# Optimization experiments

Hardware: AMD Instinct MI355X
Metric: run time of the kernel (lower is better)

Reference implementation:

```python
import jax, jax.numpy as jnp
import numpy as np

B, S, E = 2, 2048, 1024
H = 16
D = E // H
LAYER_IDX = 2.0
MASKED_BIAS = -10000.0


def setup_inputs() -> dict:
    key = jax.random.key(0)
    k1, k2, k3 = jax.random.split(key, 3)
    hidden_state = jax.random.normal(k1, (B, S, E), dtype=jnp.float32)
    w_attn = jax.random.normal(k2, (E, 3 * E), dtype=jnp.float32) * 0.2
    b_attn = jnp.zeros((3 * E,), dtype=jnp.float32)
    w_proj = jax.random.normal(k3, (E, E), dtype=jnp.float32) * 0.2
    b_proj = jnp.zeros((E,), dtype=jnp.float32)
    return {"hidden_state": hidden_state, "w_attn": w_attn, "b_attn": b_attn,
            "w_proj": w_proj, "b_proj": b_proj}


def reference(hidden_state, w_attn, b_attn, w_proj, b_proj):
    b, s, e = hidden_state.shape
    # c_attn: Conv1D == x @ W + b, then split into q, k, v
    qkv = hidden_state @ w_attn + b_attn          # [b, s, 3E]
    q, k, v = jnp.split(qkv, 3, axis=-1)
    # split heads -> [b, H, s, D]
    def split_heads(t):
        return t.reshape(b, s, H, D).transpose(0, 2, 1, 3)
    q, k, v = split_heads(q), split_heads(k), split_heads(v)
    # QK^T scaled by sqrt(d_head) then by layer_idx
    scores = jnp.einsum("bhqd,bhkd->bhqk", q, k)
    scores = scores / jnp.asarray(D ** 0.5, scores.dtype)
    scores = scores / LAYER_IDX
    # causal mask with masked_bias fill (-10000.0), matching bias buffer slice
    causal = jnp.tril(jnp.ones((s, s), dtype=bool))  # [s, s]
    scores = jnp.where(causal[None, None, :, :], scores, jnp.asarray(MASKED_BIAS, scores.dtype))
    attn = jax.nn.softmax(scores, axis=-1)
    out = jnp.einsum("bhqk,bhkd->bhqd", attn, v)   # [b, H, s, D]
    # merge heads
    out = out.transpose(0, 2, 1, 3).reshape(b, s, e)
    # c_proj
    return out @ w_proj + b_proj
```

## Files before the change

kernel.cpp:

```cpp
#include <hip/hip_runtime.h>
#include <cstddef>
#include <cstdint>

#define B_DIM   2
#define S_LEN   2048
#define EMB     1024
#define NH      16
#define HD      64
#define QKV_N   3072
#define MROWS   (B_DIM * S_LEN)

using half8  = __attribute__((ext_vector_type(8))) _Float16;
using half4  = __attribute__((ext_vector_type(4))) _Float16;
using f32x4  = __attribute__((ext_vector_type(4))) float;

#if defined(__has_builtin)
#if __has_builtin(__builtin_amdgcn_global_load_lds)
#define HAS_GLL 1
#endif
#endif

__device__ __forceinline__ void stage16(const _Float16* g, _Float16* lds_base, int lane)
{
#ifdef HAS_GLL
    (void)lane;
    __builtin_amdgcn_global_load_lds(
        (const __attribute__((address_space(1))) unsigned int*)g,
        (__attribute__((address_space(3))) unsigned int*)lds_base, 16, 0, 0);
#else
    *(half8*)(lds_base + lane * 8) = *(const half8*)g;
#endif
}

__global__ __launch_bounds__(256)
void cast_f32_f16(const float* __restrict__ src, _Float16* __restrict__ dst)
{
    int i = (blockIdx.x * 256 + threadIdx.x) * 4;
    float4 v = *(const float4*)(src + i);
    half4 h = { (_Float16)v.x, (_Float16)v.y, (_Float16)v.z, (_Float16)v.w };
    *(half4*)(dst + i) = h;
}

__global__ __launch_bounds__(256)
void transpose_cast(const float* __restrict__ W, _Float16* __restrict__ Wt,
                    int K, int N)
{
    __shared__ float T[32][33];
    const int n0 = blockIdx.x * 32, k0 = blockIdx.y * 32;
    const int t = threadIdx.x;
    const int r = t >> 3, c4 = (t & 7) * 4;
    float4 w = *(const float4*)(W + (size_t)(k0 + r) * N + n0 + c4);
    T[r][c4 + 0] = w.x; T[r][c4 + 1] = w.y;
    T[r][c4 + 2] = w.z; T[r][c4 + 3] = w.w;
    __syncthreads();
    half4 h = { (_Float16)T[c4 + 0][r], (_Float16)T[c4 + 1][r],
                (_Float16)T[c4 + 2][r], (_Float16)T[c4 + 3][r] };
    *(half4*)(Wt + (size_t)(n0 + r) * K + k0 + c4) = h;
}

__global__ __launch_bounds__(256)
void transpose_v(const _Float16* __restrict__ qkv, _Float16* __restrict__ vt)
{
    __shared__ _Float16 T[64][66];
    const int st = blockIdx.x, bh = blockIdx.y;
    const int b = bh >> 4, h = bh & 15;
    const int t = threadIdx.x;
    const int sr = t >> 2, dc = (t & 3) * 16;

    const _Float16* src = qkv + ((size_t)(b * S_LEN + st * 64 + sr)) * QKV_N
                              + 2 * EMB + h * HD + dc;
    half8 v0 = *(const half8*)(src);
    half8 v1 = *(const half8*)(src + 8);
#pragma unroll
    for (int j = 0; j < 8; ++j) { T[sr][dc + j] = v0[j]; T[sr][dc + 8 + j] = v1[j]; }
    __syncthreads();

    const int dr = t >> 2, sc = (t & 3) * 16;
    half8 o0, o1;
#pragma unroll
    for (int j = 0; j < 8; ++j) { o0[j] = T[sc + j][dr]; o1[j] = T[sc + 8 + j][dr]; }
    _Float16* dst = vt + (size_t)bh * HD * S_LEN + (size_t)dr * S_LEN + st * 64 + sc;
    *(half8*)(dst)     = o0;
    *(half8*)(dst + 8) = o1;
}

template <int MT, int MINW, bool OUT_F16>
__global__ __launch_bounds__(256, MINW)
void hgemm_lds(const _Float16* __restrict__ X, const _Float16* __restrict__ Wt,
               const float* __restrict__ bias, void* __restrict__ Cout,
               int M, int N, int K)
{
    constexpr int BM = MT * 32;
    constexpr int CA = BM / 64;
    __shared__ _Float16 As[BM][32];
    __shared__ _Float16 Bs[128][32];

    const int tid  = threadIdx.x;
    const int wave = tid >> 6, lane = tid & 63;
    const int quad = lane >> 4, l15 = lane & 15;
    const int wm = (wave >> 1) * (MT * 16);
    const int wn = (wave & 1) * 64;
    const int m0 = blockIdx.y * BM, n0 = blockIdx.x * 128;

    const int lrow = lane >> 2;
    const int lcol = (lane & 3) * 8;

    const _Float16* xg[CA];
#pragma unroll
    for (int t = 0; t < CA; ++t)
        xg[t] = X + (size_t)(m0 + t * 64 + wave * 16 + lrow) * K + lcol;
    const _Float16* wg[2];
#pragma unroll
    for (int t = 0; t < 2; ++t)
        wg[t] = Wt + (size_t)(n0 + t * 64 + wave * 16 + lrow) * K + lcol;

    f32x4 acc[MT][4] = {};

    for (int k0 = 0; k0 < K; k0 += 32) {
#pragma unroll
        for (int t = 0; t < CA; ++t)
            stage16(xg[t] + k0, &As[t * 64 + wave * 16][0], lane);
#pragma unroll
        for (int t = 0; t < 2; ++t)
            stage16(wg[t] + k0, &Bs[t * 64 + wave * 16][0], lane);
        __syncthreads();

        half8 af[MT], bf[4];
#pragma unroll
        for (int mt = 0; mt < MT; ++mt)
            af[mt] = *(const half8*)&As[wm + mt * 16 + l15][quad * 8];
#pragma unroll
        for (int nt = 0; nt < 4; ++nt)
            bf[nt] = *(const half8*)&Bs[wn + nt * 16 + l15][quad * 8];
#pragma unroll
        for (int mt = 0; mt < MT; ++mt)
#pragma unroll
            for (int nt = 0; nt < 4; ++nt)
                acc[mt][nt] = __builtin_amdgcn_mfma_f32_16x16x32_f16(
                    af[mt], bf[nt], acc[mt][nt], 0, 0, 0);
        __syncthreads();
    }

#pragma unroll
    for (int nt = 0; nt < 4; ++nt) {
        const int c = n0 + wn + nt * 16 + l15;
        const float bv = bias[c];
#pragma unroll
        for (int mt = 0; mt < MT; ++mt)
#pragma unroll
            for (int reg = 0; reg < 4; ++reg) {
                const int r = m0 + wm + mt * 16 + quad * 4 + reg;
                const float v = acc[mt][nt][reg] + bv;
                if (OUT_F16)
                    ((_Float16*)Cout)[(size_t)r * N + c] = (_Float16)v;
                else
                    ((float*)Cout)[(size_t)r * N + c] = v;
            }
    }
}

__global__ __launch_bounds__(256, 4)
void attn_fa_mfma4(const _Float16* __restrict__ qkv,
                   const _Float16* __restrict__ vt,
                   _Float16* __restrict__ outh)
{
    __shared__ _Float16 Ks[128][72];
    __shared__ _Float16 Vs[64][136];

    const int n    = blockIdx.x;
    const int half = n >> 9, idx = n & 511;
    const int bh   = idx >> 4, jj = idx & 15;
    const int qt   = half ? (31 - jj) : jj;
    const int b = bh >> 4, h = bh & 15;

    const int tid  = threadIdx.x;
    const int wave = tid >> 6, lane = tid & 63;
    const int quad = lane >> 4, l15 = lane & 15;
    const size_t row0 = (size_t)b * S_LEN;

    const _Float16 qscale = (_Float16)0.0901684400555602f;
    half8 qf[2];
    {
        const size_t qrow = row0 + qt * 64 + wave * 16 + l15;
        const _Float16* qp = qkv + qrow * QKV_N + h * HD + quad * 8;
#pragma unroll
        for (int c = 0; c < 2; ++c) {
            half8 q = *(const half8*)(qp + c * 32);
#pragma unroll
            for (int j = 0; j < 8; ++j) q[j] = q[j] * qscale;
            qf[c] = q;
        }
    }

    f32x4 o_acc[4] = {};
    float m_i = -1e30f, l_i = 0.0f;

    const int ksr = tid >> 1, ksc = (tid & 1) * 32;
    const int vsr = tid >> 2, vsc = (tid & 3) * 32;
    const _Float16* vbase = vt + (size_t)bh * HD * S_LEN;

    const int ktN = (qt + 2) >> 1;
    for (int kt = 0; kt < ktN; ++kt) {
        __syncthreads();
        {
            const _Float16* ksrc = qkv + (row0 + kt * 128 + ksr) * QKV_N
                                       + EMB + h * HD + ksc;
            half8 k0 = *(const half8*)(ksrc);
            half8 k1 = *(const half8*)(ksrc + 8);
            half8 k2 = *(const half8*)(ksrc + 16);
            half8 k3 = *(const half8*)(ksrc + 24);
            *(half8*)&Ks[ksr][ksc]      = k0;
            *(half8*)&Ks[ksr][ksc + 8]  = k1;
            *(half8*)&Ks[ksr][ksc + 16] = k2;
            *(half8*)&Ks[ksr][ksc + 24] = k3;
            const _Float16* vsrc = vbase + (size_t)vsr * S_LEN + kt * 128 + vsc;
            half8 v0 = *(const half8*)(vsrc);
            half8 v1 = *(const half8*)(vsrc + 8);
            half8 v2 = *(const half8*)(vsrc + 16);
            half8 v3 = *(const half8*)(vsrc + 24);
            *(half8*)&Vs[vsr][vsc]      = v0;
            *(half8*)&Vs[vsr][vsc + 8]  = v1;
            *(half8*)&Vs[vsr][vsc + 16] = v2;
            *(half8*)&Vs[vsr][vsc + 24] = v3;
        }
        __syncthreads();

        f32x4 st[8] = {};
#pragma unroll
        for (int c = 0; c < 2; ++c)
#pragma unroll
            for (int nt = 0; nt < 8; ++nt) {
                half8 kf = *(const half8*)&Ks[nt * 16 + l15][c * 32 + quad * 8];
                st[nt] = __builtin_amdgcn_mfma_f32_16x16x32_f16(kf, qf[c], st[nt], 0, 0, 0);
            }

        if (kt == ktN - 1) {
            const int q = qt * 64 + wave * 16 + l15;
#pragma unroll
            for (int nt = 0; nt < 8; ++nt) {
                const int ks = kt * 128 + nt * 16 + quad * 4;
#pragma unroll
                for (int reg = 0; reg < 4; ++reg)
                    if (ks + reg > q) st[nt][reg] = -1e30f;
            }
        }

        float rm = fmaxf(fmaxf(st[0][0], st[0][1]), fmaxf(st[0][2], st[0][3]));
#pragma unroll
        for (int nt = 1; nt < 8; ++nt) {
            rm = fmaxf(rm, fmaxf(st[nt][0], st[nt][1]));
            rm = fmaxf(rm, fmaxf(st[nt][2], st[nt][3]));
        }
        rm = fmaxf(rm, __shfl_xor(rm, 16));
        rm = fmaxf(rm, __shfl_xor(rm, 32));
        const float mnew  = fmaxf(m_i, rm);
        const float alpha = __builtin_amdgcn_exp2f(m_i - mnew);
        float rs = 0.0f;
        half4 pf[8];
#pragma unroll
        for (int nt = 0; nt < 8; ++nt) {
            float p0 = __builtin_amdgcn_exp2f(st[nt][0] - mnew);
            float p1 = __builtin_amdgcn_exp2f(st[nt][1] - mnew);
            float p2 = __builtin_amdgcn_exp2f(st[nt][2] - mnew);
            float p3 = __builtin_amdgcn_exp2f(st[nt][3] - mnew);
            rs += (p0 + p1) + (p2 + p3);
            pf[nt] = half4{ (_Float16)p0, (_Float16)p1, (_Float16)p2, (_Float16)p3 };
        }
        rs += __shfl_xor(rs, 16);
        rs += __shfl_xor(rs, 32);
        l_i = l_i * alpha + rs;
        m_i = mnew;
#pragma unroll
        for (int dt = 0; dt < 4; ++dt)
#pragma unroll
            for (int reg = 0; reg < 4; ++reg) o_acc[dt][reg] *= alpha;

#pragma unroll
        for (int nt = 0; nt < 8; ++nt)
#pragma unroll
            for (int dt = 0; dt < 4; ++dt) {
                half4 vf = *(const half4*)&Vs[dt * 16 + l15][nt * 16 + quad * 4];
                o_acc[dt] = __builtin_amdgcn_mfma_f32_16x16x16f16(vf, pf[nt], o_acc[dt], 0, 0, 0);
            }
    }

    const float inv = 1.0f / l_i;
    const size_t r = row0 + qt * 64 + wave * 16 + l15;
#pragma unroll
    for (int dt = 0; dt < 4; ++dt) {
        half4 o = { (_Float16)(o_acc[dt][0] * inv), (_Float16)(o_acc[dt][1] * inv),
                    (_Float16)(o_acc[dt][2] * inv), (_Float16)(o_acc[dt][3] * inv) };
        *(half4*)(outh + r * EMB + h * HD + dt * 16 + quad * 4) = o;
    }
}

extern "C" void kernel_launch(void* const* d_in, const int* in_sizes, int n_in,
                              void* d_out, int out_size, void* d_ws, size_t ws_size,
                              hipStream_t stream)
{
    const float* hidden = (const float*)d_in[0];
    const float* w_attn = (const float*)d_in[1];
    const float* b_attn = (const float*)d_in[2];
    const float* w_proj = (const float*)d_in[3];
    const float* b_proj = (const float*)d_in[4];

    _Float16* hidden_h = (_Float16*)d_ws;
    _Float16* wattn_t  = hidden_h + (size_t)MROWS * EMB;
    _Float16* wproj_t  = wattn_t + (size_t)EMB * QKV_N;
    _Float16* qkv_h    = wproj_t + (size_t)EMB * EMB;
    _Float16* attn_h   = qkv_h + (size_t)MROWS * QKV_N;
    _Float16* vt       = attn_h + (size_t)MROWS * EMB;

    cast_f32_f16<<<(MROWS * EMB) / 1024, 256, 0, stream>>>(hidden, hidden_h);
    transpose_cast<<<dim3(QKV_N / 32, EMB / 32), 256, 0, stream>>>(
        w_attn, wattn_t, EMB, QKV_N);
    transpose_cast<<<dim3(EMB / 32, EMB / 32), 256, 0, stream>>>(
        w_proj, wproj_t, EMB, EMB);

    hgemm_lds<4, 3, true><<<dim3(QKV_N / 128, MROWS / 128), 256, 0, stream>>>(
        hidden_h, wattn_t, b_attn, qkv_h, MROWS, QKV_N, EMB);

    transpose_v<<<dim3(S_LEN / 64, B_DIM * NH), 256, 0, stream>>>(qkv_h, vt);

    attn_fa_mfma4<<<dim3(1024), 256, 0, stream>>>(qkv_h, vt, attn_h);

    hgemm_lds<2, 4, false><<<dim3(EMB / 128, MROWS / 64), 256, 0, stream>>>(
        attn_h, wproj_t, b_proj, d_out, MROWS, EMB, EMB);
}
```

Measured before the change: 203.3 us.

## Use XOR-swizzled LDS with direct global-to-LDS staging in GEMM and attention

The GEMM now stages a K=64 slice per iteration into an XOR-swizzled LDS layout, which halves the number of barrier pairs and avoids bank conflicts without padding. The attention kernel replaces its register-staged, padded K/V tiles with swizzled unpadded tiles loaded through the stage16 global-to-LDS path. It also skips the online-softmax rescale when no lane's running max grows. This adds index arithmetic, and the swizzle patterns must match stage16's lane mapping exactly or results will be wrong.

```diff
diff --git a/kernel.cpp b/kernel.cpp
--- a/kernel.cpp
+++ b/kernel.cpp
@@ -91,9 +91,9 @@
                int M, int N, int K)
 {
     constexpr int BM = MT * 32;
-    constexpr int CA = BM / 64;
-    __shared__ _Float16 As[BM][32];
-    __shared__ _Float16 Bs[128][32];
+    constexpr int ACALLS = BM / 32;
+    __shared__ _Float16 As[BM][64];
+    __shared__ _Float16 Bs[128][64];
 
     const int tid  = threadIdx.x;
     const int wave = tid >> 6, lane = tid & 63;
@@ -102,42 +102,46 @@
     const int wn = (wave & 1) * 64;
     const int m0 = blockIdx.y * BM, n0 = blockIdx.x * 128;
 
-    const int lrow = lane >> 2;
-    const int lcol = (lane & 3) * 8;
-
-    const _Float16* xg[CA];
-#pragma unroll
-    for (int t = 0; t < CA; ++t)
-        xg[t] = X + (size_t)(m0 + t * 64 + wave * 16 + lrow) * K + lcol;
-    const _Float16* wg[2];
-#pragma unroll
-    for (int t = 0; t < 2; ++t)
-        wg[t] = Wt + (size_t)(n0 + t * 64 + wave * 16 + lrow) * K + lcol;
+    const int srow = lane >> 3;
+    const int scol = ((lane & 7) ^ srow) * 8;
+
+    const _Float16* xg[ACALLS];
+#pragma unroll
+    for (int c = 0; c < ACALLS; ++c)
+        xg[c] = X + (size_t)(m0 + wave * (BM / 4) + c * 8 + srow) * K + scol;
+    const _Float16* wg[4];
+#pragma unroll
+    for (int c = 0; c < 4; ++c)
+        wg[c] = Wt + (size_t)(n0 + wave * 32 + c * 8 + srow) * K + scol;
 
     f32x4 acc[MT][4] = {};
-
-    for (int k0 = 0; k0 < K; k0 += 32) {
-#pragma unroll
-        for (int t = 0; t < CA; ++t)
-            stage16(xg[t] + k0, &As[t * 64 + wave * 16][0], lane);
-#pragma unroll
-        for (int t = 0; t < 2; ++t)
-            stage16(wg[t] + k0, &Bs[t * 64 + wave * 16][0], lane);
+    const int sx = l15 & 7;
+
+    for (int k0 = 0; k0 < K; k0 += 64) {
+#pragma unroll
+        for (int c = 0; c < ACALLS; ++c)
+            stage16(xg[c] + k0, &As[wave * (BM / 4) + c * 8][0], lane);
+#pragma unroll
+        for (int c = 0; c < 4; ++c)
+            stage16(wg[c] + k0, &Bs[wave * 32 + c * 8][0], lane);
         __syncthreads();
 
-        half8 af[MT], bf[4];
-#pragma unroll
-        for (int mt = 0; mt < MT; ++mt)
-            af[mt] = *(const half8*)&As[wm + mt * 16 + l15][quad * 8];
-#pragma unroll
-        for (int nt = 0; nt < 4; ++nt)
-            bf[nt] = *(const half8*)&Bs[wn + nt * 16 + l15][quad * 8];
-#pragma unroll
-        for (int mt = 0; mt < MT; ++mt)
+#pragma unroll
+        for (int cc = 0; cc < 2; ++cc) {
+            half8 af[MT], bf[4];
+#pragma unroll
+            for (int mt = 0; mt < MT; ++mt)
+                af[mt] = *(const half8*)&As[wm + mt * 16 + l15][(((cc * 4 + quad) ^ sx)) * 8];
 #pragma unroll
             for (int nt = 0; nt < 4; ++nt)
-                acc[mt][nt] = __builtin_amdgcn_mfma_f32_16x16x32_f16(
-                    af[mt], bf[nt], acc[mt][nt], 0, 0, 0);
+                bf[nt] = *(const half8*)&Bs[wn + nt * 16 + l15][(((cc * 4 + quad) ^ sx)) * 8];
+#pragma unroll
+            for (int mt = 0; mt < MT; ++mt)
+#pragma unroll
+                for (int nt = 0; nt < 4; ++nt)
+                    acc[mt][nt] = __builtin_amdgcn_mfma_f32_16x16x32_f16(
+                        af[mt], bf[nt], acc[mt][nt], 0, 0, 0);
+        }
         __syncthreads();
     }
 
@@ -160,12 +164,12 @@
 }
 
 __global__ __launch_bounds__(256, 4)
-void attn_fa_mfma4(const _Float16* __restrict__ qkv,
+void attn_fa_mfma5(const _Float16* __restrict__ qkv,
                    const _Float16* __restrict__ vt,
                    _Float16* __restrict__ outh)
 {
-    __shared__ _Float16 Ks[128][72];
-    __shared__ _Float16 Vs[64][136];
+    __shared__ _Float16 Ks[128][64];
+    __shared__ _Float16 Vs[64][128];
 
     const int n    = blockIdx.x;
     const int half = n >> 9, idx = n & 511;
@@ -195,33 +199,30 @@
     f32x4 o_acc[4] = {};
     float m_i = -1e30f, l_i = 0.0f;
 
-    const int ksr = tid >> 1, ksc = (tid & 1) * 32;
-    const int vsr = tid >> 2, vsc = (tid & 3) * 32;
+    const int ksrow = lane >> 3;
+    const int kscol = ((lane & 7) ^ ksrow) * 8;
+    const int vsrow = lane >> 4;
     const _Float16* vbase = vt + (size_t)bh * HD * S_LEN;
+    const int sxk = l15 & 7;
 
     const int ktN = (qt + 2) >> 1;
     for (int kt = 0; kt < ktN; ++kt) {
         __syncthreads();
         {
-            const _Float16* ksrc = qkv + (row0 + kt * 128 + ksr) * QKV_N
-                                       + EMB + h * HD + ksc;
-            half8 k0 = *(const half8*)(ksrc);
-            half8 k1 = *(const half8*)(ksrc + 8);
-            half8 k2 = *(const half8*)(ksrc + 16);
-            half8 k3 = *(const half8*)(ksrc + 24);
-            *(half8*)&Ks[ksr][ksc]      = k0;
-            *(half8*)&Ks[ksr][ksc + 8]  = k1;
-            *(half8*)&Ks[ksr][ksc + 16] = k2;
-            *(half8*)&Ks[ksr][ksc + 24] = k3;
-            const _Float16* vsrc = vbase + (size_t)vsr * S_LEN + kt * 128 + vsc;
-            half8 v0 = *(const half8*)(vsrc);
-            half8 v1 = *(const half8*)(vsrc + 8);
-            half8 v2 = *(const half8*)(vsrc + 16);
-            half8 v3 = *(const half8*)(vsrc + 24);
-            *(half8*)&Vs[vsr][vsc]      = v0;
-            *(half8*)&Vs[vsr][vsc + 8]  = v1;
-            *(half8*)&Vs[vsr][vsc + 16] = v2;
-            *(half8*)&Vs[vsr][vsc + 24] = v3;
+            const _Float16* kbase = qkv + (row0 + kt * 128) * QKV_N + EMB + h * HD;
+#pragma unroll
+            for (int c = 0; c < 4; ++c) {
+                const int r0 = wave * 32 + c * 8;
+                stage16(kbase + (size_t)(r0 + ksrow) * QKV_N + kscol,
+                        &Ks[r0][0], lane);
+            }
+#pragma unroll
+            for (int c = 0; c < 4; ++c) {
+                const int r0 = wave * 16 + c * 4;
+                const int sgv = ((lane & 15) ^ (c * 4 + vsrow)) * 8;
+                stage16(vbase + (size_t)(r0 + vsrow) * S_LEN + kt * 128 + sgv,
+                        &Vs[r0][0], lane);
+            }
         }
         __syncthreads();
 
@@ -230,7 +231,7 @@
         for (int c = 0; c < 2; ++c)
 #pragma unroll
             for (int nt = 0; nt < 8; ++nt) {
-                half8 kf = *(const half8*)&Ks[nt * 16 + l15][c * 32 + quad * 8];
+                half8 kf = *(const half8*)&Ks[nt * 16 + l15][((c * 4 + quad) ^ sxk) * 8];
                 st[nt] = __builtin_amdgcn_mfma_f32_16x16x32_f16(kf, qf[c], st[nt], 0, 0, 0);
             }
 
@@ -253,8 +254,18 @@
         }
         rm = fmaxf(rm, __shfl_xor(rm, 16));
         rm = fmaxf(rm, __shfl_xor(rm, 32));
-        const float mnew  = fmaxf(m_i, rm);
-        const float alpha = __builtin_amdgcn_exp2f(m_i - mnew);
+        const float mnew = fmaxf(m_i, rm);
+
+        if (__ballot(mnew > m_i)) {
+            const float alpha = __builtin_amdgcn_exp2f(m_i - mnew);
+            l_i *= alpha;
+#pragma unroll
+            for (int dt = 0; dt < 4; ++dt)
+#pragma unroll
+                for (int reg = 0; reg < 4; ++reg) o_acc[dt][reg] *= alpha;
+        }
+        m_i = mnew;
+
         float rs = 0.0f;
         half4 pf[8];
 #pragma unroll
@@ -268,18 +279,14 @@
         }
         rs += __shfl_xor(rs, 16);
         rs += __shfl_xor(rs, 32);
-        l_i = l_i * alpha + rs;
-        m_i = mnew;
-#pragma unroll
-        for (int dt = 0; dt < 4; ++dt)
-#pragma unroll
-            for (int reg = 0; reg < 4; ++reg) o_acc[dt][reg] *= alpha;
+        l_i += rs;
 
 #pragma unroll
         for (int nt = 0; nt < 8; ++nt)
 #pragma unroll
             for (int dt = 0; dt < 4; ++dt) {
-                half4 vf = *(const half4*)&Vs[dt * 16 + l15][nt * 16 + quad * 4];
+                const int pg = ((2 * nt + (quad >> 1)) ^ l15) * 8 + (quad & 1) * 4;
+                half4 vf = *(const half4*)&Vs[dt * 16 + l15][pg];
                 o_acc[dt] = __builtin_amdgcn_mfma_f32_16x16x16f16(vf, pf[nt], o_acc[dt], 0, 0, 0);
             }
     }
@@ -322,7 +329,7 @@
 
     transpose_v<<<dim3(S_LEN / 64, B_DIM * NH), 256, 0, stream>>>(qkv_h, vt);
 
-    attn_fa_mfma4<<<dim3(1024), 256, 0, stream>>>(qkv_h, vt, attn_h);
+    attn_fa_mfma5<<<dim3(1024), 256, 0, stream>>>(qkv_h, vt, attn_h);
 
     hgemm_lds<2, 4, false><<<dim3(EMB / 128, MROWS / 64), 256, 0, stream>>>(
         attn_h, wproj_t, b_proj, d_out, MROWS, EMB, EMB);
```

New measurement: 188.9 us. -7.1%, faster.
